# Kernel tuning notes

Hardware: AMD Instinct MI355X
Metric: run time of the kernel (lower is better)

Reference implementation:

```python
import jax, jax.numpy as jnp
import numpy as np

N = 50000      # nodes
E = 800000     # edges (before self loops)
RNA, SS, H, G = 645, 6, 128, 200
EPS = 1e-5

def setup_inputs() -> dict:
    key = jax.random.key(0)
    ks = jax.random.split(key, 16)
    def rn(k, shape, s=0.05):
        return jax.random.normal(k, shape, jnp.float32) * s
    return {
        "rna_embeddings": jax.random.normal(ks[0], (N, RNA), jnp.float32),
        "ss_emb": jax.random.normal(ks[1], (N, SS), jnp.float32),
        "edge_index": jax.random.randint(ks[2], (2, E), 0, N),
        "batch": jnp.sort(jax.random.randint(ks[3], (N,), 0, G)),
        "W_fuse": rn(ks[4], (RNA + SS, H)), "b_fuse": jnp.zeros((H,), jnp.float32),
        "ln1_g": jnp.ones((H,), jnp.float32), "ln1_b": jnp.zeros((H,), jnp.float32),
        "W_gat": rn(ks[5], (H, H)), "att_src": rn(ks[6], (H,)), "att_dst": rn(ks[7], (H,)),
        "b_gat": jnp.zeros((H,), jnp.float32),
        "gn_w": jnp.ones((H,), jnp.float32), "gn_b": jnp.zeros((H,), jnp.float32), "gn_ms": jnp.ones((H,), jnp.float32),
        "W_gate": rn(ks[8], (2 * H, H)), "b_gate": jnp.zeros((H,), jnp.float32),
        "W_head": rn(ks[9], (H, H)), "b_head": jnp.zeros((H,), jnp.float32),
        "ln2_g": jnp.ones((H,), jnp.float32), "ln2_b": jnp.zeros((H,), jnp.float32),
        "W_fc1": rn(ks[10], (H, H // 2)), "b_fc1": jnp.zeros((H // 2,), jnp.float32),
        "ln3_g": jnp.ones((H // 2,), jnp.float32), "ln3_b": jnp.zeros((H // 2,), jnp.float32),
        "W_fc2": rn(ks[11], (H // 2, 1)), "b_fc2": jnp.zeros((1,), jnp.float32),
    }

def _ln(x, g, b):
    m = jnp.mean(x, -1, keepdims=True)
    v = jnp.mean(jnp.square(x - m), -1, keepdims=True)
    return (x - m) * jax.lax.rsqrt(v + EPS) * g + b

def _graphnorm(x, batch, w, b, ms):
    cnt = jax.ops.segment_sum(jnp.ones((x.shape[0], 1), x.dtype), batch, num_segments=G)
    mean = jax.ops.segment_sum(x, batch, num_segments=G) / jnp.maximum(cnt, 1.0)
    out = x - ms * mean[batch]
    var = jax.ops.segment_sum(jnp.square(out), batch, num_segments=G) / jnp.maximum(cnt, 1.0)
    std = jnp.sqrt(var + EPS)
    return w * out / std[batch] + b

def _gat(x, src, dst, W, a_src, a_dst, bias):
    xw = x @ W                                     # [N,H]
    e = (xw @ a_src)[src] + (xw @ a_dst)[dst]      # per-edge score
    e = jax.nn.leaky_relu(e, 0.2)
    m = jax.ops.segment_max(e, dst, num_segments=N)  # every dst has a self loop
    e = jnp.exp(e - m[dst])
    s = jax.ops.segment_sum(e, dst, num_segments=N)
    alpha = e / (s[dst] + 1e-16)
    return jax.ops.segment_sum(alpha[:, None] * xw[src], dst, num_segments=N) + bias

def reference(rna_embeddings, ss_emb, edge_index, batch,
              W_fuse, b_fuse, ln1_g, ln1_b,
              W_gat, att_src, att_dst, b_gat,
              gn_w, gn_b, gn_ms,
              W_gate, b_gate, W_head, b_head, ln2_g, ln2_b,
              W_fc1, b_fc1, ln3_g, ln3_b, W_fc2, b_fc2):
    loop = jnp.arange(N)
    src = jnp.concatenate([edge_index[0], loop])   # PyG GATConv add_self_loops=True
    dst = jnp.concatenate([edge_index[1], loop])
    h = jax.nn.relu(_ln(jnp.concatenate([rna_embeddings, ss_emb], -1) @ W_fuse + b_fuse, ln1_g, ln1_b))
    h_res = h
    h = jax.nn.relu(_graphnorm(_gat(h, src, dst, W_gat, att_src, att_dst, b_gat), batch, gn_w, gn_b, gn_ms))
    h1 = h
    h = jax.nn.relu(_graphnorm(_gat(h1, src, dst, W_gat, att_src, att_dst, b_gat), batch, gn_w, gn_b, gn_ms))
    h2 = h + h_res
    gate = jax.nn.sigmoid(jnp.concatenate([h1, h2], -1) @ W_gate + b_gate)
    h = gate * h1 + (1.0 - gate) * h2
    h = jax.nn.relu(_ln(h @ W_head + b_head, ln2_g, ln2_b))
    h = jax.nn.relu(_ln(h @ W_fc1 + b_fc1, ln3_g, ln3_b))
    return (h @ W_fc2 + b_fc2)[:, 0]
```

## Files before the change

kernel.cpp:

```cpp
#include <hip/hip_runtime.h>
#include <hip/hip_bf16.h>
#include <math.h>

#define NN 50000
#define EE 800000
#define RNA_D 645
#define KFUSE 651
#define KPACK 704
#define HD 128
#define GG 200
#define SAK 72
#define HGS 136

typedef __attribute__((ext_vector_type(8))) short shortx8;
typedef __attribute__((ext_vector_type(4))) float floatx4;

__device__ __forceinline__ float lrelu(float x){ return x >= 0.f ? x : 0.2f*x; }
__device__ __forceinline__ short f2bf(float x){
  union { __hip_bfloat16 h; short s; } u; u.h = __float2bfloat16(x); return u.s;
}
__device__ __forceinline__ float bf2f(short s){
  union { float f; unsigned u; } c; c.u = ((unsigned)(unsigned short)s) << 16; return c.f;
}
__device__ __forceinline__ float2 upk(unsigned u){
  union { float f; unsigned v; } a, b;
  a.v = u << 16; b.v = u & 0xffff0000u;
  return make_float2(a.f, b.f);
}

__launch_bounds__(256)
__global__ void pack_kernel(const float* __restrict__ rna, const float* __restrict__ ss,
                            short* __restrict__ Abf){
  int row = blockIdx.x*2 + (threadIdx.x >> 7);
  int t = threadIdx.x & 127;
  if (row >= NN) return;
  const float* rrow = rna + (size_t)row*RNA_D;
  short* orow = Abf + (size_t)row*KPACK;
  #pragma unroll
  for (int j=0;j<6;++j){
    int c = t + j*128;
    if (c < KPACK){
      float v = 0.f;
      if (c < RNA_D) v = rrow[c];
      else if (c < KFUSE) v = ss[row*6 + (c - RNA_D)];
      orow[c] = f2bf(v);
    }
  }
}

__global__ void hist_gstart_kernel(const int* __restrict__ dst, int* __restrict__ deg,
                                   const int* __restrict__ batch, int* __restrict__ gstart){
  int e = blockIdx.x*256 + threadIdx.x;
  if (e < EE) atomicAdd(&deg[dst[e]], 1);
  if (e < NN){
    int g = batch[e];
    if (e == 0){ for (int gg=0; gg<=g; ++gg) gstart[gg] = 0; }
    else { int gp = batch[e-1]; for (int gg=gp+1; gg<=g; ++gg) gstart[gg] = e; }
    if (e == NN-1){ for (int gg=g+1; gg<=GG; ++gg) gstart[gg] = NN; }
  }
}
__global__ void scan1_kernel(const int* __restrict__ deg, int* __restrict__ row_start,
                             int* __restrict__ blocksum){
  __shared__ int s[256];
  int i = blockIdx.x*256 + threadIdx.x;
  int v = (i < NN) ? deg[i] : 0;
  s[threadIdx.x] = v;
  __syncthreads();
  for (int off=1; off<256; off<<=1){
    int t = (threadIdx.x >= off) ? s[threadIdx.x-off] : 0;
    __syncthreads();
    s[threadIdx.x] += t;
    __syncthreads();
  }
  if (i < NN) row_start[i] = s[threadIdx.x] - v;
  if (threadIdx.x == 255) blocksum[blockIdx.x] = s[255];
}
__global__ void scan2_kernel(int* __restrict__ blocksum, int nb){
  __shared__ int s[256];
  int v = (threadIdx.x < nb) ? blocksum[threadIdx.x] : 0;
  s[threadIdx.x] = v;
  __syncthreads();
  for (int off=1; off<256; off<<=1){
    int t = (threadIdx.x >= off) ? s[threadIdx.x-off] : 0;
    __syncthreads();
    s[threadIdx.x] += t;
    __syncthreads();
  }
  blocksum[threadIdx.x] = s[threadIdx.x] - v;
}
__global__ void scan3_kernel(int* __restrict__ row_start, const int* __restrict__ blocksum,
                             int* __restrict__ cursor){
  int i = blockIdx.x*256 + threadIdx.x;
  if (i < NN){
    int v = row_start[i] + blocksum[blockIdx.x];
    row_start[i] = v;
    cursor[i] = v;
  }
  if (i == 0) row_start[NN] = EE;
}
__global__ void scatter_kernel(const int* __restrict__ srcl, const int* __restrict__ dstl,
                               int* __restrict__ cursor, int* __restrict__ csr_src){
  int e = blockIdx.x*256 + threadIdx.x;
  if (e >= EE) return;
  int d = dstl[e];
  int slot = atomicAdd(&cursor[d], 1);
  csr_src[slot] = srcl[e];
}

__global__ void wprep_all_kernel(const float* __restrict__ Wf, const float* __restrict__ Wg,
                                 const float* __restrict__ Wgt, const float* __restrict__ Wh,
                                 const float* __restrict__ W1,
                                 short* __restrict__ Tf, short* __restrict__ Tg,
                                 short* __restrict__ Tgt, short* __restrict__ Th,
                                 short* __restrict__ T1){
  int idx = blockIdx.x*256 + threadIdx.x;
  const int S0=128*KPACK, S1=128*128, S2=128*256, S3=128*128, S4=64*128;
  if (idx < S0){ int n=idx/KPACK, k=idx-n*KPACK; Tf[idx]=f2bf(k<KFUSE ? Wf[k*128+n] : 0.f); return; }
  idx -= S0;
  if (idx < S1){ int n=idx>>7, k=idx&127; Tg[idx]=f2bf(Wg[k*128+n]); return; }
  idx -= S1;
  if (idx < S2){ int n=idx>>8, k=idx&255; Tgt[idx]=f2bf(Wgt[k*128+n]); return; }
  idx -= S2;
  if (idx < S3){ int n=idx>>7, k=idx&127; Th[idx]=f2bf(Wh[k*128+n]); return; }
  idx -= S3;
  if (idx < S4){ int n=idx>>7, k=idx&127; T1[idx]=f2bf(W1[k*64+n]); return; }
}

template<int MODE, int NT, bool GNA>
__launch_bounds__(256)
__global__ void mfma_gemm(const float* __restrict__ A0,
                          const short* __restrict__ Apk,
                          const short* __restrict__ Wt, const float* __restrict__ bias,
                          const float* __restrict__ gw, const float* __restrict__ gb,
                          const float* __restrict__ as_, const float* __restrict__ ad_,
                          const int* __restrict__ batch, const float* __restrict__ gnsh,
                          const float* __restrict__ gnsc, float* __restrict__ side,
                          float* __restrict__ out, short* __restrict__ outb,
                          float* __restrict__ es, float* __restrict__ ed,
                          int K, int Kp){
  __shared__ short sA[128*SAK];
  __shared__ short sB[NT*16*SAK];
  const int tid  = threadIdx.x;
  const int wave = tid >> 6, lane = tid & 63;
  const int quad = lane >> 4, l16 = lane & 15;
  const int rowBase = blockIdx.x * 128;
  const int NCOL = NT*16;

  floatx4 acc[2][NT];
  #pragma unroll
  for (int t=0;t<2;++t)
    #pragma unroll
    for (int ct=0;ct<NT;++ct)
      #pragma unroll
      for (int j=0;j<4;++j) acc[t][ct][j] = 0.f;

  const int srow = tid >> 1, shalf = tid & 1;
  const int sgr = rowBase + srow;

  for (int k0 = 0; k0 < K; k0 += 64){
    if (MODE == 0){
      #pragma unroll
      for (int j=0;j<4;++j){
        int flat = tid + j*256;
        int r = flat >> 3, c8 = flat & 7;
        int gr = rowBase + r;
        shortx8 v = {0,0,0,0,0,0,0,0};
        if (gr < NN) v = *(const shortx8*)&Apk[(size_t)gr*KPACK + k0 + c8*8];
        *(shortx8*)&sA[r*SAK + c8*8] = v;
      }
    } else {
      int kb = k0 + shalf*32;
      short tmp[32];
      if (GNA){
        int g = (sgr < NN) ? batch[sgr] : 0;
        const float* py  = A0 + (size_t)sgr*HD + kb;
        const float* psh = gnsh + g*HD + kb;
        const float* psc = gnsc + g*HD + kb;
        const float* pbb = gb + kb;
        #pragma unroll
        for (int q4=0;q4<8;++q4){
          float4 yv = (sgr < NN) ? *(const float4*)(py + q4*4) : make_float4(0.f,0.f,0.f,0.f);
          float4 sh = *(const float4*)(psh + q4*4);
          float4 sc = *(const float4*)(psc + q4*4);
          float4 bb = *(const float4*)(pbb + q4*4);
          float4 v;
          v.x = fmaxf((yv.x - sh.x)*sc.x + bb.x, 0.f);
          v.y = fmaxf((yv.y - sh.y)*sc.y + bb.y, 0.f);
          v.z = fmaxf((yv.z - sh.z)*sc.z + bb.z, 0.f);
          v.w = fmaxf((yv.w - sh.w)*sc.w + bb.w, 0.f);
          if (sgr < NN) *(float4*)&side[(size_t)sgr*HD + kb + q4*4] = v;
          tmp[q4*4+0]=f2bf(v.x); tmp[q4*4+1]=f2bf(v.y);
          tmp[q4*4+2]=f2bf(v.z); tmp[q4*4+3]=f2bf(v.w);
        }
      } else {
        const float* p = A0 + (size_t)sgr*HD + kb;
        #pragma unroll
        for (int q4=0;q4<8;++q4){
          float4 f = (sgr < NN) ? *(const float4*)(p + q4*4) : make_float4(0.f,0.f,0.f,0.f);
          tmp[q4*4+0]=f2bf(f.x); tmp[q4*4+1]=f2bf(f.y);
          tmp[q4*4+2]=f2bf(f.z); tmp[q4*4+3]=f2bf(f.w);
        }
      }
      #pragma unroll
      for (int q8=0;q8<4;++q8)
        *(shortx8*)&sA[srow*SAK + shalf*32 + q8*8] = *(shortx8*)&tmp[q8*8];
    }
    {
      int col = tid >> 1, kb = k0 + (tid&1)*32;
      #pragma unroll
      for (int q8=0;q8<4;++q8)
        *(shortx8*)&sB[col*SAK + (tid&1)*32 + q8*8] = *(const shortx8*)&Wt[(size_t)col*Kp + kb + q8*8];
    }
    __syncthreads();
    #pragma unroll
    for (int ks=0; ks<2; ++ks){
      int kb = ks*32 + quad*8;
      shortx8 af0 = *(const shortx8*)&sA[(wave*32 +      l16)*SAK + kb];
      shortx8 af1 = *(const shortx8*)&sA[(wave*32 + 16 + l16)*SAK + kb];
      #pragma unroll
      for (int ct=0; ct<NT; ++ct){
        shortx8 bf = *(const shortx8*)&sB[(ct*16 + l16)*SAK + kb];
        acc[0][ct] = __builtin_amdgcn_mfma_f32_16x16x32_bf16(af0, bf, acc[0][ct], 0,0,0);
        acc[1][ct] = __builtin_amdgcn_mfma_f32_16x16x32_bf16(af1, bf, acc[1][ct], 0,0,0);
      }
    }
    __syncthreads();
  }

  if (MODE == 1){
    float asv[NT], adv[NT];
    #pragma unroll
    for (int ct=0;ct<NT;++ct){ asv[ct] = as_[ct*16+l16]; adv[ct] = ad_[ct*16+l16]; }
    #pragma unroll
    for (int t=0;t<2;++t)
      #pragma unroll
      for (int i=0;i<4;++i){
        int gr = rowBase + wave*32 + t*16 + quad*4 + i;
        float s=0.f, d=0.f;
        #pragma unroll
        for (int ct=0;ct<NT;++ct){
          float v = acc[t][ct][i];
          s = fmaf(v, asv[ct], s); d = fmaf(v, adv[ct], d);
          if (gr < NN) outb[(size_t)gr*HD + ct*16 + l16] = f2bf(v);
        }
        #pragma unroll
        for (int off=1; off<16; off<<=1){ s += __shfl_xor(s,off); d += __shfl_xor(d,off); }
        if (l16 == 0 && gr < NN){ es[gr] = s; ed[gr] = d; }
      }
  } else {
    float biasv[NT], gv[NT], bv[NT];
    #pragma unroll
    for (int ct=0;ct<NT;++ct){
      biasv[ct] = bias[ct*16+l16]; gv[ct] = gw[ct*16+l16]; bv[ct] = gb[ct*16+l16];
    }
    #pragma unroll
    for (int t=0;t<2;++t)
      #pragma unroll
      for (int i=0;i<4;++i){
        int gr = rowBase + wave*32 + t*16 + quad*4 + i;
        float v[NT]; float s=0.f, q=0.f;
        #pragma unroll
        for (int ct=0;ct<NT;++ct){
          v[ct] = acc[t][ct][i] + biasv[ct];
          s += v[ct]; q = fmaf(v[ct], v[ct], q);
        }
        #pragma unroll
        for (int off=1; off<16; off<<=1){ s += __shfl_xor(s,off); q += __shfl_xor(q,off); }
        float mean = s * (1.f/NCOL);
        float inv  = rsqrtf(q*(1.f/NCOL) - mean*mean + 1e-5f);
        if (gr < NN){
          #pragma unroll
          for (int ct=0;ct<NT;++ct)
            out[(size_t)gr*NCOL + ct*16 + l16] = fmaxf((v[ct]-mean)*inv*gv[ct] + bv[ct], 0.f);
        }
      }
  }
}

__launch_bounds__(256)
__global__ void gat_aggregate_kernel(const short* __restrict__ xwb, const float* __restrict__ es,
                                     const float* __restrict__ ed, const int* __restrict__ row_start,
                                     const int* __restrict__ csr_src, const float* __restrict__ bgat,
                                     float* __restrict__ out){
  int gid = blockIdx.x*256 + threadIdx.x;
  int n = gid >> 6, lane = gid & 63;
  if (n >= NN) return;
  int beg = row_start[n], end = row_start[n+1];
  float edn = ed[n];
  float sc_self = lrelu(es[n] + edn);

  int i0 = beg + lane;
  bool v0 = i0 < end;
  int sA = v0 ? csr_src[i0] : 0;
  float eA = v0 ? lrelu(es[sA] + edn) : -3.0e38f;
  float m = fmaxf(sc_self, eA);
  for (int i = beg + 64 + lane; i < end; i += 64)
    m = fmaxf(m, lrelu(es[csr_src[i]] + edn));
  #pragma unroll
  for (int off=1; off<64; off<<=1) m = fmaxf(m, __shfl_xor(m, off));

  float wA = v0 ? __expf(eA - m) : 0.f;
  float wsum_l = wA;
  float wself = __expf(sc_self - m);
  float2 self2 = upk(*(const unsigned*)&xwb[(size_t)n*HD + 2*lane]);
  float a0 = wself*self2.x, a1 = wself*self2.y;

  int deg0 = min(end - beg, 64);
  int j = 0;
  for (; j + 8 <= deg0; j += 8){
    int ss[8]; float ww[8]; unsigned xv[8];
    #pragma unroll
    for (int u=0;u<8;++u){ ss[u]=__shfl(sA,j+u); ww[u]=__shfl(wA,j+u); }
    #pragma unroll
    for (int u=0;u<8;++u) xv[u] = *(const unsigned*)&xwb[(size_t)ss[u]*HD + 2*lane];
    #pragma unroll
    for (int u=0;u<8;++u){ float2 f=upk(xv[u]); a0=fmaf(ww[u],f.x,a0); a1=fmaf(ww[u],f.y,a1); }
  }
  for (; j < deg0; ++j){
    int s=__shfl(sA,j); float w=__shfl(wA,j);
    float2 f = upk(*(const unsigned*)&xwb[(size_t)s*HD + 2*lane]);
    a0=fmaf(w,f.x,a0); a1=fmaf(w,f.y,a1);
  }
  for (int c = beg + 64; c < end; c += 64){
    int i = c + lane;
    bool vb = i < end;
    int sB = vb ? csr_src[i] : 0;
    float wB = vb ? __expf(lrelu(es[sB] + edn) - m) : 0.f;
    wsum_l += wB;
    int degc = min(end - c, 64);
    for (int jj=0; jj<degc; ++jj){
      int s=__shfl(sB,jj); float w=__shfl(wB,jj);
      float2 f = upk(*(const unsigned*)&xwb[(size_t)s*HD + 2*lane]);
      a0=fmaf(w,f.x,a0); a1=fmaf(w,f.y,a1);
    }
  }
  #pragma unroll
  for (int off=1; off<64; off<<=1) wsum_l += __shfl_xor(wsum_l, off);
  float dinv = 1.f/(wsum_l + wself + 1e-16f);
  float2 b2 = *(const float2*)&bgat[2*lane];
  float2 o; o.x = a0*dinv + b2.x; o.y = a1*dinv + b2.y;
  *(float2*)&out[(size_t)n*HD + 2*lane] = o;
}

__launch_bounds__(256)
__global__ void gn_group_kernel(const float* __restrict__ x, const int* __restrict__ gstart,
                                const float* __restrict__ gnw, const float* __restrict__ gnms,
                                float* __restrict__ shiftv, float* __restrict__ scalev){
  int g = blockIdx.x;
  int n0 = gstart[g], n1 = gstart[g+1];
  int f = threadIdx.x & 127, half = threadIdx.x >> 7;
  float s = 0.f, q = 0.f;
  for (int n = n0 + half; n < n1; n += 2){
    float v = x[(size_t)n*HD + f];
    s += v; q = fmaf(v, v, q);
  }
  __shared__ float rs[256], rq[256];
  rs[threadIdx.x] = s; rq[threadIdx.x] = q;
  __syncthreads();
  if (threadIdx.x < 128){
    s = rs[threadIdx.x] + rs[threadIdx.x+128];
    q = rq[threadIdx.x] + rq[threadIdx.x+128];
    float c = fmaxf((float)(n1 - n0), 1.f);
    float mean = s / c;
    float ms = gnms[f];
    float var = q/c - mean*mean*ms*(2.f - ms);
    shiftv[g*HD+f] = ms*mean;
    scalev[g*HD+f] = gnw[f] / sqrtf(var + 1e-5f);
  }
}

__launch_bounds__(256)
__global__ void tail_kernel(const float* __restrict__ h1, const float* __restrict__ y2,
                            const float* __restrict__ hres, const int* __restrict__ batch,
                            const float* __restrict__ gnsh, const float* __restrict__ gnsc,
                            const float* __restrict__ gnb,
                            const short* __restrict__ Wt_gate, const float* __restrict__ b_gate,
                            const short* __restrict__ Wt_head, const float* __restrict__ b_head,
                            const float* __restrict__ ln2g, const float* __restrict__ ln2b,
                            const short* __restrict__ Wt_fc1, const float* __restrict__ b_fc1,
                            const float* __restrict__ ln3g, const float* __restrict__ ln3b,
                            const float* __restrict__ W_fc2, const float* __restrict__ b_fc2,
                            float* __restrict__ outp){
  __shared__ short hgL[128*HGS];
  __shared__ short sA[128*SAK];
  __shared__ short sB[128*SAK];
  const int tid = threadIdx.x, wave = tid>>6, lane = tid&63;
  const int quad = lane>>4, l16 = lane&15;
  const int rowBase = blockIdx.x*128;
  const int srow = tid>>1, shalf = tid&1;
  const int sgr = rowBase + srow;

  floatx4 acc[2][8];
  #pragma unroll
  for (int t=0;t<2;++t)
    #pragma unroll
    for (int ct=0;ct<8;++ct)
      #pragma unroll
      for (int j=0;j<4;++j) acc[t][ct][j]=0.f;

  for (int c2=0; c2<4; ++c2){
    int kb = c2*64 + shalf*32;
    short tmp[32];
    if (kb < 128){
      const float* p = h1 + (size_t)sgr*HD + kb;
      #pragma unroll
      for (int q4=0;q4<8;++q4){
        float4 f = (sgr < NN) ? *(const float4*)(p + q4*4) : make_float4(0.f,0.f,0.f,0.f);
        tmp[q4*4+0]=f2bf(f.x); tmp[q4*4+1]=f2bf(f.y);
        tmp[q4*4+2]=f2bf(f.z); tmp[q4*4+3]=f2bf(f.w);
      }
    } else {
      int cb = kb - 128;
      int g = (sgr < NN) ? batch[sgr] : 0;
      const float* py  = y2   + (size_t)sgr*HD + cb;
      const float* ph  = hres + (size_t)sgr*HD + cb;
      const float* psh = gnsh + g*HD + cb;
      const float* psc = gnsc + g*HD + cb;
      const float* pbb = gnb + cb;
      #pragma unroll
      for (int q4=0;q4<8;++q4){
        float4 yv = (sgr < NN) ? *(const float4*)(py + q4*4) : make_float4(0.f,0.f,0.f,0.f);
        float4 hv = (sgr < NN) ? *(const float4*)(ph + q4*4) : make_float4(0.f,0.f,0.f,0.f);
        float4 sh = *(const float4*)(psh + q4*4);
        float4 sc = *(const float4*)(psc + q4*4);
        float4 bb = *(const float4*)(pbb + q4*4);
        float4 v;
        v.x = fmaxf((yv.x - sh.x)*sc.x + bb.x, 0.f) + hv.x;
        v.y = fmaxf((yv.y - sh.y)*sc.y + bb.y, 0.f) + hv.y;
        v.z = fmaxf((yv.z - sh.z)*sc.z + bb.z, 0.f) + hv.z;
        v.w = fmaxf((yv.w - sh.w)*sc.w + bb.w, 0.f) + hv.w;
        tmp[q4*4+0]=f2bf(v.x); tmp[q4*4+1]=f2bf(v.y);
        tmp[q4*4+2]=f2bf(v.z); tmp[q4*4+3]=f2bf(v.w);
      }
      #pragma unroll
      for (int q8=0;q8<4;++q8)
        *(shortx8*)&hgL[srow*HGS + cb + q8*8] = *(shortx8*)&tmp[q8*8];
    }
    #pragma unroll
    for (int q8=0;q8<4;++q8)
      *(shortx8*)&sA[srow*SAK + shalf*32 + q8*8] = *(shortx8*)&tmp[q8*8];
    {
      int col = tid >> 1, kb2 = c2*64 + (tid&1)*32;
      #pragma unroll
      for (int q8=0;q8<4;++q8)
        *(shortx8*)&sB[col*SAK + (tid&1)*32 + q8*8] = *(const shortx8*)&Wt_gate[(size_t)col*256 + kb2 + q8*8];
    }
    __syncthreads();
    #pragma unroll
    for (int ks=0; ks<2; ++ks){
      int kk = ks*32 + quad*8;
      shortx8 af0 = *(const shortx8*)&sA[(wave*32 +      l16)*SAK + kk];
      shortx8 af1 = *(const shortx8*)&sA[(wave*32 + 16 + l16)*SAK + kk];
      #pragma unroll
      for (int ct=0; ct<8; ++ct){
        shortx8 bf = *(const shortx8*)&sB[(ct*16 + l16)*SAK + kk];
        acc[0][ct] = __builtin_amdgcn_mfma_f32_16x16x32_bf16(af0, bf, acc[0][ct], 0,0,0);
        acc[1][ct] = __builtin_amdgcn_mfma_f32_16x16x32_bf16(af1, bf, acc[1][ct], 0,0,0);
      }
    }
    __syncthreads();
  }
  {
    float biasv[8];
    #pragma unroll
    for (int ct=0;ct<8;++ct) biasv[ct] = b_gate[ct*16+l16];
    #pragma unroll
    for (int t=0;t<2;++t)
      #pragma unroll
      for (int i=0;i<4;++i){
        int row = wave*32 + t*16 + quad*4 + i;
        int gr = rowBase + row;
        #pragma unroll
        for (int ct=0;ct<8;++ct){
          int c = ct*16 + l16;
          float g = 1.f/(1.f + __expf(-(acc[t][ct][i] + biasv[ct])));
          float x1 = (gr < NN) ? h1[(size_t)gr*HD + c] : 0.f;
          float x2 = bf2f(hgL[row*HGS + c]);
          hgL[row*HGS + c] = f2bf(g*x1 + (1.f-g)*x2);
        }
      }
  }
  __syncthreads();

  floatx4 acc2[2][8];
  #pragma unroll
  for (int t=0;t<2;++t)
    #pragma unroll
    for (int ct=0;ct<8;++ct)
      #pragma unroll
      for (int j=0;j<4;++j) acc2[t][ct][j]=0.f;
  for (int c2=0;c2<2;++c2){
    {
      int col = tid >> 1, kb2 = c2*64 + (tid&1)*32;
      #pragma unroll
      for (int q8=0;q8<4;++q8)
        *(shortx8*)&sB[col*SAK + (tid&1)*32 + q8*8] = *(const shortx8*)&Wt_head[(size_t)col*128 + kb2 + q8*8];
    }
    __syncthreads();
    #pragma unroll
    for (int ks=0; ks<2; ++ks){
      int kg = c2*64 + ks*32 + quad*8;
      int kk = ks*32 + quad*8;
      shortx8 af0 = *(const shortx8*)&hgL[(wave*32 +      l16)*HGS + kg];
      shortx8 af1 = *(const shortx8*)&hgL[(wave*32 + 16 + l16)*HGS + kg];
      #pragma unroll
      for (int ct=0; ct<8; ++ct){
        shortx8 bf = *(const shortx8*)&sB[(ct*16 + l16)*SAK + kk];
        acc2[0][ct] = __builtin_amdgcn_mfma_f32_16x16x32_bf16(af0, bf, acc2[0][ct], 0,0,0);
        acc2[1][ct] = __builtin_amdgcn_mfma_f32_16x16x32_bf16(af1, bf, acc2[1][ct], 0,0,0);
      }
    }
    __syncthreads();
  }
  {
    float biasv[8], gv[8], bv[8];
    #pragma unroll
    for (int ct=0;ct<8;++ct){
      biasv[ct] = b_head[ct*16+l16]; gv[ct] = ln2g[ct*16+l16]; bv[ct] = ln2b[ct*16+l16];
    }
    #pragma unroll
    for (int t=0;t<2;++t)
      #pragma unroll
      for (int i=0;i<4;++i){
        int row = wave*32 + t*16 + quad*4 + i;
        float v[8]; float s=0.f, q=0.f;
        #pragma unroll
        for (int ct=0;ct<8;++ct){
          v[ct] = acc2[t][ct][i] + biasv[ct];
          s += v[ct]; q = fmaf(v[ct], v[ct], q);
        }
        #pragma unroll
        for (int off=1; off<16; off<<=1){ s += __shfl_xor(s,off); q += __shfl_xor(q,off); }
        float mean = s * (1.f/128.f);
        float inv  = rsqrtf(q*(1.f/128.f) - mean*mean + 1e-5f);
        #pragma unroll
        for (int ct=0;ct<8;++ct)
          hgL[row*HGS + ct*16 + l16] = f2bf(fmaxf((v[ct]-mean)*inv*gv[ct] + bv[ct], 0.f));
      }
  }
  __syncthreads();

  floatx4 acc3[2][4];
  #pragma unroll
  for (int t=0;t<2;++t)
    #pragma unroll
    for (int ct=0;ct<4;++ct)
      #pragma unroll
      for (int j=0;j<4;++j) acc3[t][ct][j]=0.f;
  for (int c2=0;c2<2;++c2){
    if (tid < 128){
      int col = tid >> 1, kb2 = c2*64 + (tid&1)*32;
      #pragma unroll
      for (int q8=0;q8<4;++q8)
        *(shortx8*)&sB[col*SAK + (tid&1)*32 + q8*8] = *(const shortx8*)&Wt_fc1[(size_t)col*128 + kb2 + q8*8];
    }
    __syncthreads();
    #pragma unroll
    for (int ks=0; ks<2; ++ks){
      int kg = c2*64 + ks*32 + quad*8;
      int kk = ks*32 + quad*8;
      shortx8 af0 = *(const shortx8*)&hgL[(wave*32 +      l16)*HGS + kg];
      shortx8 af1 = *(const shortx8*)&hgL[(wave*32 + 16 + l16)*HGS + kg];
      #pragma unroll
      for (int ct=0; ct<4; ++ct){
        shortx8 bf = *(const shortx8*)&sB[(ct*16 + l16)*SAK + kk];
        acc3[0][ct] = __builtin_amdgcn_mfma_f32_16x16x32_bf16(af0, bf, acc3[0][ct], 0,0,0);
        acc3[1][ct] = __builtin_amdgcn_mfma_f32_16x16x32_bf16(af1, bf, acc3[1][ct], 0,0,0);
      }
    }
    __syncthreads();
  }
  {
    float biasv[4], gv[4], bv[4], w2v[4];
    #pragma unroll
    for (int ct=0;ct<4;++ct){
      biasv[ct] = b_fc1[ct*16+l16]; gv[ct] = ln3g[ct*16+l16]; bv[ct] = ln3b[ct*16+l16];
      w2v[ct] = W_fc2[ct*16+l16];
    }
    float b2 = b_fc2[0];
    #pragma unroll
    for (int t=0;t<2;++t)
      #pragma unroll
      for (int i=0;i<4;++i){
        int gr = rowBase + wave*32 + t*16 + quad*4 + i;
        float v[4]; float s=0.f, q=0.f;
        #pragma unroll
        for (int ct=0;ct<4;++ct){
          v[ct] = acc3[t][ct][i] + biasv[ct];
          s += v[ct]; q = fmaf(v[ct], v[ct], q);
        }
        #pragma unroll
        for (int off=1; off<16; off<<=1){ s += __shfl_xor(s,off); q += __shfl_xor(q,off); }
        float mean = s * (1.f/64.f);
        float inv  = rsqrtf(q*(1.f/64.f) - mean*mean + 1e-5f);
        float p = 0.f;
        #pragma unroll
        for (int ct=0;ct<4;++ct){
          float o = fmaxf((v[ct]-mean)*inv*gv[ct] + bv[ct], 0.f);
          p = fmaf(o, w2v[ct], p);
        }
        #pragma unroll
        for (int off=1; off<16; off<<=1) p += __shfl_xor(p, off);
        if (l16 == 0 && gr < NN) outp[gr] = p + b2;
      }
  }
}

extern "C" void kernel_launch(void* const* d_in, const int* in_sizes, int n_in,
                              void* d_out, int out_size, void* d_ws, size_t ws_size,
                              hipStream_t stream){
  const float* rna    = (const float*)d_in[0];
  const float* ss     = (const float*)d_in[1];
  const int*   eidx   = (const int*)d_in[2];
  const int*   batch  = (const int*)d_in[3];
  const float* W_fuse = (const float*)d_in[4];
  const float* b_fuse = (const float*)d_in[5];
  const float* ln1_g  = (const float*)d_in[6];
  const float* ln1_b  = (const float*)d_in[7];
  const float* W_gat  = (const float*)d_in[8];
  const float* att_src= (const float*)d_in[9];
  const float* att_dst= (const float*)d_in[10];
  const float* b_gat  = (const float*)d_in[11];
  const float* gn_w   = (const float*)d_in[12];
  const float* gn_b   = (const float*)d_in[13];
  const float* gn_ms  = (const float*)d_in[14];
  const float* W_gate = (const float*)d_in[15];
  const float* b_gate = (const float*)d_in[16];
  const float* W_head = (const float*)d_in[17];
  const float* b_head = (const float*)d_in[18];
  const float* ln2_g  = (const float*)d_in[19];
  const float* ln2_b  = (const float*)d_in[20];
  const float* W_fc1  = (const float*)d_in[21];
  const float* b_fc1  = (const float*)d_in[22];
  const float* ln3_g  = (const float*)d_in[23];
  const float* ln3_b  = (const float*)d_in[24];
  const float* W_fc2  = (const float*)d_in[25];
  const float* b_fc2  = (const float*)d_in[26];
  float* outp = (float*)d_out;

  const int* srcl = eidx;
  const int* dstl = eidx + EE;

  char* base = (char*)d_ws;
  size_t off = 0;
  auto alloc = [&](size_t bytes)->void*{
    void* p = base + off; off = (off + bytes + 255) & ~(size_t)255; return p;
  };
  float* h    = (float*)alloc((size_t)NN*HD*4);
  float* h1   = (float*)alloc((size_t)NN*HD*4);
  float* y    = (float*)alloc((size_t)NN*HD*4);
  short* xwb  = (short*)alloc((size_t)NN*HD*2);
  float* es   = (float*)alloc((size_t)NN*4);
  float* ed   = (float*)alloc((size_t)NN*4);
  float* shiftv = (float*)alloc(GG*HD*4);
  float* scalev = (float*)alloc(GG*HD*4);
  int* deg       = (int*)alloc((size_t)NN*4);
  int* row_start = (int*)alloc((size_t)(NN+1)*4);
  int* cursor    = (int*)alloc((size_t)NN*4);
  int* csr_src   = (int*)alloc((size_t)EE*4);
  int* blocksum  = (int*)alloc(256*4);
  int* gstart    = (int*)alloc((GG+1)*4);
  short* Abf     = (short*)alloc((size_t)NN*KPACK*2);
  short* Wt_fuse = (short*)alloc((size_t)128*KPACK*2);
  short* Wt_gat  = (short*)alloc((size_t)128*128*2);
  short* Wt_gate = (short*)alloc((size_t)128*256*2);
  short* Wt_head = (short*)alloc((size_t)128*128*2);
  short* Wt_fc1  = (short*)alloc((size_t)64*128*2);

  const int NB  = (NN + 255)/256;
  const int GB  = (NN + 127)/128;
  const int EB  = (EE + 255)/256;
  const int WVB = (NN*64 + 255)/256;
  const int WPREP_TOT = 128*KPACK + 128*128 + 128*256 + 128*128 + 64*128;

  pack_kernel<<<(NN+1)/2, 256, 0, stream>>>(rna, ss, Abf);
  wprep_all_kernel<<<(WPREP_TOT+255)/256, 256, 0, stream>>>(
      W_fuse, W_gat, W_gate, W_head, W_fc1,
      Wt_fuse, Wt_gat, Wt_gate, Wt_head, Wt_fc1);

  hipMemsetAsync(deg, 0, (size_t)NN*4, stream);
  hist_gstart_kernel<<<EB, 256, 0, stream>>>(dstl, deg, batch, gstart);
  scan1_kernel<<<NB, 256, 0, stream>>>(deg, row_start, blocksum);
  scan2_kernel<<<1, 256, 0, stream>>>(blocksum, NB);
  scan3_kernel<<<NB, 256, 0, stream>>>(row_start, blocksum, cursor);
  scatter_kernel<<<EB, 256, 0, stream>>>(srcl, dstl, cursor, csr_src);

  mfma_gemm<0,8,false><<<GB, 256, 0, stream>>>(nullptr, Abf, Wt_fuse, b_fuse, ln1_g, ln1_b,
      nullptr, nullptr, nullptr, nullptr, nullptr, nullptr, h, nullptr, nullptr, nullptr, KPACK, KPACK);

  mfma_gemm<1,8,false><<<GB, 256, 0, stream>>>(h, nullptr, Wt_gat, nullptr, nullptr, nullptr,
      att_src, att_dst, nullptr, nullptr, nullptr, nullptr, nullptr, xwb, es, ed, HD, HD);
  gat_aggregate_kernel<<<WVB, 256, 0, stream>>>(xwb, es, ed, row_start, csr_src, b_gat, y);
  gn_group_kernel<<<GG, 256, 0, stream>>>(y, gstart, gn_w, gn_ms, shiftv, scalev);

  mfma_gemm<1,8,true><<<GB, 256, 0, stream>>>(y, nullptr, Wt_gat, nullptr, nullptr, gn_b,
      att_src, att_dst, batch, shiftv, scalev, h1, nullptr, xwb, es, ed, HD, HD);
  gat_aggregate_kernel<<<WVB, 256, 0, stream>>>(xwb, es, ed, row_start, csr_src, b_gat, y);
  gn_group_kernel<<<GG, 256, 0, stream>>>(y, gstart, gn_w, gn_ms, shiftv, scalev);

  tail_kernel<<<GB, 256, 0, stream>>>(h1, y, h, batch, shiftv, scalev, gn_b,
      Wt_gate, b_gate, Wt_head, b_head, ln2_g, ln2_b,
      Wt_fc1, b_fc1, ln3_g, ln3_b, W_fc2, b_fc2, outp);
}
```

Measured before the change: 623.9 us.

## Fuse input packing into fuse GEMM, store hidden states in bf16, merge scans

Drops the separate pack kernel. The fuse GEMM now reads the fp32 rna/ss inputs directly and converts them to bf16 while staging into shared memory. This removes a full write and re-read of a large packed bf16 matrix. The hidden states h and h1 are stored as bf16 instead of fp32 and consumed in bf16 by the xW GEMM and the tail kernel, which halves their traffic at some cost in precision for the residual path. The three-kernel degree scan becomes a single 1024-thread block, and the GAT aggregation tail loops are processed in padded groups of 8 gathers instead of one at a time.

```diff
diff --git a/kernel.cpp b/kernel.cpp
--- a/kernel.cpp
+++ b/kernel.cpp
@@ -28,26 +28,6 @@
   return make_float2(a.f, b.f);
 }
 
-__launch_bounds__(256)
-__global__ void pack_kernel(const float* __restrict__ rna, const float* __restrict__ ss,
-                            short* __restrict__ Abf){
-  int row = blockIdx.x*2 + (threadIdx.x >> 7);
-  int t = threadIdx.x & 127;
-  if (row >= NN) return;
-  const float* rrow = rna + (size_t)row*RNA_D;
-  short* orow = Abf + (size_t)row*KPACK;
-  #pragma unroll
-  for (int j=0;j<6;++j){
-    int c = t + j*128;
-    if (c < KPACK){
-      float v = 0.f;
-      if (c < RNA_D) v = rrow[c];
-      else if (c < KFUSE) v = ss[row*6 + (c - RNA_D)];
-      orow[c] = f2bf(v);
-    }
-  }
-}
-
 __global__ void hist_gstart_kernel(const int* __restrict__ dst, int* __restrict__ deg,
                                    const int* __restrict__ batch, int* __restrict__ gstart){
   int e = blockIdx.x*256 + threadIdx.x;
@@ -59,44 +39,25 @@
     if (e == NN-1){ for (int gg=g+1; gg<=GG; ++gg) gstart[gg] = NN; }
   }
 }
-__global__ void scan1_kernel(const int* __restrict__ deg, int* __restrict__ row_start,
-                             int* __restrict__ blocksum){
-  __shared__ int s[256];
-  int i = blockIdx.x*256 + threadIdx.x;
-  int v = (i < NN) ? deg[i] : 0;
-  s[threadIdx.x] = v;
+__launch_bounds__(1024)
+__global__ void scan_all_kernel(const int* __restrict__ deg, int* __restrict__ row_start,
+                                int* __restrict__ cursor){
+  __shared__ int s[1024];
+  int t = threadIdx.x;
+  int b0 = t*49, b1 = min(b0+49, NN);
+  int sum = 0;
+  for (int i=b0;i<b1;++i) sum += deg[i];
+  s[t] = sum;
   __syncthreads();
-  for (int off=1; off<256; off<<=1){
-    int t = (threadIdx.x >= off) ? s[threadIdx.x-off] : 0;
-    __syncthreads();
-    s[threadIdx.x] += t;
-    __syncthreads();
-  }
-  if (i < NN) row_start[i] = s[threadIdx.x] - v;
-  if (threadIdx.x == 255) blocksum[blockIdx.x] = s[255];
-}
-__global__ void scan2_kernel(int* __restrict__ blocksum, int nb){
-  __shared__ int s[256];
-  int v = (threadIdx.x < nb) ? blocksum[threadIdx.x] : 0;
-  s[threadIdx.x] = v;
-  __syncthreads();
-  for (int off=1; off<256; off<<=1){
-    int t = (threadIdx.x >= off) ? s[threadIdx.x-off] : 0;
-    __syncthreads();
-    s[threadIdx.x] += t;
-    __syncthreads();
-  }
-  blocksum[threadIdx.x] = s[threadIdx.x] - v;
-}
-__global__ void scan3_kernel(int* __restrict__ row_start, const int* __restrict__ blocksum,
-                             int* __restrict__ cursor){
-  int i = blockIdx.x*256 + threadIdx.x;
-  if (i < NN){
-    int v = row_start[i] + blocksum[blockIdx.x];
-    row_start[i] = v;
-    cursor[i] = v;
-  }
-  if (i == 0) row_start[NN] = EE;
+  for (int off=1; off<1024; off<<=1){
+    int v = (t>=off) ? s[t-off] : 0;
+    __syncthreads();
+    s[t] += v;
+    __syncthreads();
+  }
+  int pre = (t==0) ? 0 : s[t-1];
+  for (int i=b0;i<b1;++i){ int d=deg[i]; row_start[i]=pre; cursor[i]=pre; pre+=d; }
+  if (t==0) row_start[NN] = EE;
 }
 __global__ void scatter_kernel(const int* __restrict__ srcl, const int* __restrict__ dstl,
                                int* __restrict__ cursor, int* __restrict__ csr_src){
@@ -126,90 +87,45 @@
   if (idx < S4){ int n=idx>>7, k=idx&127; T1[idx]=f2bf(W1[k*64+n]); return; }
 }
 
-template<int MODE, int NT, bool GNA>
 __launch_bounds__(256)
-__global__ void mfma_gemm(const float* __restrict__ A0,
-                          const short* __restrict__ Apk,
-                          const short* __restrict__ Wt, const float* __restrict__ bias,
-                          const float* __restrict__ gw, const float* __restrict__ gb,
-                          const float* __restrict__ as_, const float* __restrict__ ad_,
-                          const int* __restrict__ batch, const float* __restrict__ gnsh,
-                          const float* __restrict__ gnsc, float* __restrict__ side,
-                          float* __restrict__ out, short* __restrict__ outb,
-                          float* __restrict__ es, float* __restrict__ ed,
-                          int K, int Kp){
+__global__ void fuse_gemm_kernel(const float* __restrict__ rna, const float* __restrict__ ss,
+                                 const short* __restrict__ Wt, const float* __restrict__ bias,
+                                 const float* __restrict__ gw, const float* __restrict__ gb,
+                                 short* __restrict__ hb){
   __shared__ short sA[128*SAK];
-  __shared__ short sB[NT*16*SAK];
+  __shared__ short sB[128*SAK];
   const int tid  = threadIdx.x;
   const int wave = tid >> 6, lane = tid & 63;
   const int quad = lane >> 4, l16 = lane & 15;
   const int rowBase = blockIdx.x * 128;
-  const int NCOL = NT*16;
-
-  floatx4 acc[2][NT];
+
+  floatx4 acc[2][8];
   #pragma unroll
   for (int t=0;t<2;++t)
     #pragma unroll
-    for (int ct=0;ct<NT;++ct)
+    for (int ct=0;ct<8;++ct)
       #pragma unroll
       for (int j=0;j<4;++j) acc[t][ct][j] = 0.f;
 
-  const int srow = tid >> 1, shalf = tid & 1;
-  const int sgr = rowBase + srow;
-
-  for (int k0 = 0; k0 < K; k0 += 64){
-    if (MODE == 0){
-      #pragma unroll
-      for (int j=0;j<4;++j){
-        int flat = tid + j*256;
-        int r = flat >> 3, c8 = flat & 7;
-        int gr = rowBase + r;
-        shortx8 v = {0,0,0,0,0,0,0,0};
-        if (gr < NN) v = *(const shortx8*)&Apk[(size_t)gr*KPACK + k0 + c8*8];
-        *(shortx8*)&sA[r*SAK + c8*8] = v;
-      }
-    } else {
-      int kb = k0 + shalf*32;
-      short tmp[32];
-      if (GNA){
-        int g = (sgr < NN) ? batch[sgr] : 0;
-        const float* py  = A0 + (size_t)sgr*HD + kb;
-        const float* psh = gnsh + g*HD + kb;
-        const float* psc = gnsc + g*HD + kb;
-        const float* pbb = gb + kb;
-        #pragma unroll
-        for (int q4=0;q4<8;++q4){
-          float4 yv = (sgr < NN) ? *(const float4*)(py + q4*4) : make_float4(0.f,0.f,0.f,0.f);
-          float4 sh = *(const float4*)(psh + q4*4);
-          float4 sc = *(const float4*)(psc + q4*4);
-          float4 bb = *(const float4*)(pbb + q4*4);
-          float4 v;
-          v.x = fmaxf((yv.x - sh.x)*sc.x + bb.x, 0.f);
-          v.y = fmaxf((yv.y - sh.y)*sc.y + bb.y, 0.f);
-          v.z = fmaxf((yv.z - sh.z)*sc.z + bb.z, 0.f);
-          v.w = fmaxf((yv.w - sh.w)*sc.w + bb.w, 0.f);
-          if (sgr < NN) *(float4*)&side[(size_t)sgr*HD + kb + q4*4] = v;
-          tmp[q4*4+0]=f2bf(v.x); tmp[q4*4+1]=f2bf(v.y);
-          tmp[q4*4+2]=f2bf(v.z); tmp[q4*4+3]=f2bf(v.w);
-        }
-      } else {
-        const float* p = A0 + (size_t)sgr*HD + kb;
-        #pragma unroll
-        for (int q4=0;q4<8;++q4){
-          float4 f = (sgr < NN) ? *(const float4*)(p + q4*4) : make_float4(0.f,0.f,0.f,0.f);
-          tmp[q4*4+0]=f2bf(f.x); tmp[q4*4+1]=f2bf(f.y);
-          tmp[q4*4+2]=f2bf(f.z); tmp[q4*4+3]=f2bf(f.w);
-        }
-      }
+  const int rsub = tid >> 6;
+  const int col  = tid & 63;
+
+  for (int k0 = 0; k0 < KPACK; k0 += 64){
+    #pragma unroll
+    for (int i=0;i<32;++i){
+      int row = i*4 + rsub;
+      int gr = rowBase + row;
+      int gk = k0 + col;
+      float v = 0.f;
+      if (gr < NN && gk < KFUSE)
+        v = (gk < RNA_D) ? rna[(size_t)gr*RNA_D + gk] : ss[gr*6 + (gk - RNA_D)];
+      sA[row*SAK + col] = f2bf(v);
+    }
+    {
+      int bcol = tid >> 1, kb = k0 + (tid&1)*32;
       #pragma unroll
       for (int q8=0;q8<4;++q8)
-        *(shortx8*)&sA[srow*SAK + shalf*32 + q8*8] = *(shortx8*)&tmp[q8*8];
-    }
-    {
-      int col = tid >> 1, kb = k0 + (tid&1)*32;
-      #pragma unroll
-      for (int q8=0;q8<4;++q8)
-        *(shortx8*)&sB[col*SAK + (tid&1)*32 + q8*8] = *(const shortx8*)&Wt[(size_t)col*Kp + kb + q8*8];
+        *(shortx8*)&sB[bcol*SAK + (tid&1)*32 + q8*8] = *(const shortx8*)&Wt[(size_t)bcol*KPACK + kb + q8*8];
     }
     __syncthreads();
     #pragma unroll
@@ -218,7 +134,7 @@
       shortx8 af0 = *(const shortx8*)&sA[(wave*32 +      l16)*SAK + kb];
       shortx8 af1 = *(const shortx8*)&sA[(wave*32 + 16 + l16)*SAK + kb];
       #pragma unroll
-      for (int ct=0; ct<NT; ++ct){
+      for (int ct=0; ct<8; ++ct){
         shortx8 bf = *(const shortx8*)&sB[(ct*16 + l16)*SAK + kb];
         acc[0][ct] = __builtin_amdgcn_mfma_f32_16x16x32_bf16(af0, bf, acc[0][ct], 0,0,0);
         acc[1][ct] = __builtin_amdgcn_mfma_f32_16x16x32_bf16(af1, bf, acc[1][ct], 0,0,0);
@@ -226,55 +142,138 @@
     }
     __syncthreads();
   }
-
-  if (MODE == 1){
-    float asv[NT], adv[NT];
-    #pragma unroll
-    for (int ct=0;ct<NT;++ct){ asv[ct] = as_[ct*16+l16]; adv[ct] = ad_[ct*16+l16]; }
-    #pragma unroll
-    for (int t=0;t<2;++t)
-      #pragma unroll
-      for (int i=0;i<4;++i){
-        int gr = rowBase + wave*32 + t*16 + quad*4 + i;
-        float s=0.f, d=0.f;
-        #pragma unroll
-        for (int ct=0;ct<NT;++ct){
-          float v = acc[t][ct][i];
-          s = fmaf(v, asv[ct], s); d = fmaf(v, adv[ct], d);
-          if (gr < NN) outb[(size_t)gr*HD + ct*16 + l16] = f2bf(v);
-        }
-        #pragma unroll
-        for (int off=1; off<16; off<<=1){ s += __shfl_xor(s,off); d += __shfl_xor(d,off); }
-        if (l16 == 0 && gr < NN){ es[gr] = s; ed[gr] = d; }
-      }
-  } else {
-    float biasv[NT], gv[NT], bv[NT];
-    #pragma unroll
-    for (int ct=0;ct<NT;++ct){
-      biasv[ct] = bias[ct*16+l16]; gv[ct] = gw[ct*16+l16]; bv[ct] = gb[ct*16+l16];
-    }
-    #pragma unroll
-    for (int t=0;t<2;++t)
-      #pragma unroll
-      for (int i=0;i<4;++i){
-        int gr = rowBase + wave*32 + t*16 + quad*4 + i;
-        float v[NT]; float s=0.f, q=0.f;
-        #pragma unroll
-        for (int ct=0;ct<NT;++ct){
-          v[ct] = acc[t][ct][i] + biasv[ct];
-          s += v[ct]; q = fmaf(v[ct], v[ct], q);
-        }
-        #pragma unroll
-        for (int off=1; off<16; off<<=1){ s += __shfl_xor(s,off); q += __shfl_xor(q,off); }
-        float mean = s * (1.f/NCOL);
-        float inv  = rsqrtf(q*(1.f/NCOL) - mean*mean + 1e-5f);
-        if (gr < NN){
-          #pragma unroll
-          for (int ct=0;ct<NT;++ct)
-            out[(size_t)gr*NCOL + ct*16 + l16] = fmaxf((v[ct]-mean)*inv*gv[ct] + bv[ct], 0.f);
-        }
-      }
-  }
+  float biasv[8], gv[8], bv[8];
+  #pragma unroll
+  for (int ct=0;ct<8;++ct){
+    biasv[ct] = bias[ct*16+l16]; gv[ct] = gw[ct*16+l16]; bv[ct] = gb[ct*16+l16];
+  }
+  #pragma unroll
+  for (int t=0;t<2;++t)
+    #pragma unroll
+    for (int i=0;i<4;++i){
+      int gr = rowBase + wave*32 + t*16 + quad*4 + i;
+      float v[8]; float s=0.f, q=0.f;
+      #pragma unroll
+      for (int ct=0;ct<8;++ct){
+        v[ct] = acc[t][ct][i] + biasv[ct];
+        s += v[ct]; q = fmaf(v[ct], v[ct], q);
+      }
+      #pragma unroll
+      for (int off=1; off<16; off<<=1){ s += __shfl_xor(s,off); q += __shfl_xor(q,off); }
+      float mean = s * (1.f/128.f);
+      float inv  = rsqrtf(q*(1.f/128.f) - mean*mean + 1e-5f);
+      if (gr < NN){
+        #pragma unroll
+        for (int ct=0;ct<8;++ct)
+          hb[(size_t)gr*HD + ct*16 + l16] = f2bf(fmaxf((v[ct]-mean)*inv*gv[ct] + bv[ct], 0.f));
+      }
+    }
+}
+
+template<bool GNA>
+__launch_bounds__(256)
+__global__ void xw_gemm_kernel(const short* __restrict__ Ab, const float* __restrict__ Af,
+                               const short* __restrict__ Wt,
+                               const float* __restrict__ as_, const float* __restrict__ ad_,
+                               const int* __restrict__ batch, const float* __restrict__ gnsh,
+                               const float* __restrict__ gnsc, const float* __restrict__ gnb,
+                               short* __restrict__ sideb,
+                               short* __restrict__ xwb, float* __restrict__ es, float* __restrict__ ed){
+  __shared__ short sA[128*SAK];
+  __shared__ short sB[128*SAK];
+  const int tid  = threadIdx.x;
+  const int wave = tid >> 6, lane = tid & 63;
+  const int quad = lane >> 4, l16 = lane & 15;
+  const int rowBase = blockIdx.x * 128;
+
+  floatx4 acc[2][8];
+  #pragma unroll
+  for (int t=0;t<2;++t)
+    #pragma unroll
+    for (int ct=0;ct<8;++ct)
+      #pragma unroll
+      for (int j=0;j<4;++j) acc[t][ct][j] = 0.f;
+
+  const int srow = tid >> 1, shalf = tid & 1;
+  const int sgr = rowBase + srow;
+
+  for (int k0 = 0; k0 < HD; k0 += 64){
+    int kb = k0 + shalf*32;
+    if (GNA){
+      short tmp[32];
+      int g = (sgr < NN) ? batch[sgr] : 0;
+      const float* py  = Af + (size_t)sgr*HD + kb;
+      const float* psh = gnsh + g*HD + kb;
+      const float* psc = gnsc + g*HD + kb;
+      const float* pbb = gnb + kb;
+      #pragma unroll
+      for (int q4=0;q4<8;++q4){
+        float4 yv = (sgr < NN) ? *(const float4*)(py + q4*4) : make_float4(0.f,0.f,0.f,0.f);
+        float4 sh = *(const float4*)(psh + q4*4);
+        float4 sc = *(const float4*)(psc + q4*4);
+        float4 bb = *(const float4*)(pbb + q4*4);
+        float4 v;
+        v.x = fmaxf((yv.x - sh.x)*sc.x + bb.x, 0.f);
+        v.y = fmaxf((yv.y - sh.y)*sc.y + bb.y, 0.f);
+        v.z = fmaxf((yv.z - sh.z)*sc.z + bb.z, 0.f);
+        v.w = fmaxf((yv.w - sh.w)*sc.w + bb.w, 0.f);
+        tmp[q4*4+0]=f2bf(v.x); tmp[q4*4+1]=f2bf(v.y);
+        tmp[q4*4+2]=f2bf(v.z); tmp[q4*4+3]=f2bf(v.w);
+      }
+      #pragma unroll
+      for (int q8=0;q8<4;++q8){
+        shortx8 t8 = *(shortx8*)&tmp[q8*8];
+        *(shortx8*)&sA[srow*SAK + shalf*32 + q8*8] = t8;
+        if (sgr < NN) *(shortx8*)&sideb[(size_t)sgr*HD + kb + q8*8] = t8;
+      }
+    } else {
+      #pragma unroll
+      for (int q8=0;q8<4;++q8){
+        shortx8 v = {0,0,0,0,0,0,0,0};
+        if (sgr < NN) v = *(const shortx8*)&Ab[(size_t)sgr*HD + kb + q8*8];
+        *(shortx8*)&sA[srow*SAK + shalf*32 + q8*8] = v;
+      }
+    }
+    {
+      int col = tid >> 1, kb2 = k0 + (tid&1)*32;
+      #pragma unroll
+      for (int q8=0;q8<4;++q8)
+        *(shortx8*)&sB[col*SAK + (tid&1)*32 + q8*8] = *(const shortx8*)&Wt[(size_t)col*HD + kb2 + q8*8];
+    }
+    __syncthreads();
+    #pragma unroll
+    for (int ks=0; ks<2; ++ks){
+      int kk = ks*32 + quad*8;
+      shortx8 af0 = *(const shortx8*)&sA[(wave*32 +      l16)*SAK + kk];
+      shortx8 af1 = *(const shortx8*)&sA[(wave*32 + 16 + l16)*SAK + kk];
+      #pragma unroll
+      for (int ct=0; ct<8; ++ct){
+        shortx8 bf = *(const shortx8*)&sB[(ct*16 + l16)*SAK + kk];
+        acc[0][ct] = __builtin_amdgcn_mfma_f32_16x16x32_bf16(af0, bf, acc[0][ct], 0,0,0);
+        acc[1][ct] = __builtin_amdgcn_mfma_f32_16x16x32_bf16(af1, bf, acc[1][ct], 0,0,0);
+      }
+    }
+    __syncthreads();
+  }
+  float asv[8], adv[8];
+  #pragma unroll
+  for (int ct=0;ct<8;++ct){ asv[ct] = as_[ct*16+l16]; adv[ct] = ad_[ct*16+l16]; }
+  #pragma unroll
+  for (int t=0;t<2;++t)
+    #pragma unroll
+    for (int i=0;i<4;++i){
+      int gr = rowBase + wave*32 + t*16 + quad*4 + i;
+      float s=0.f, d=0.f;
+      #pragma unroll
+      for (int ct=0;ct<8;++ct){
+        float v = acc[t][ct][i];
+        s = fmaf(v, asv[ct], s); d = fmaf(v, adv[ct], d);
+        if (gr < NN) xwb[(size_t)gr*HD + ct*16 + l16] = f2bf(v);
+      }
+      #pragma unroll
+      for (int off=1; off<16; off<<=1){ s += __shfl_xor(s,off); d += __shfl_xor(d,off); }
+      if (l16 == 0 && gr < NN){ es[gr] = s; ed[gr] = d; }
+    }
 }
 
 __launch_bounds__(256)
@@ -306,8 +305,7 @@
   float a0 = wself*self2.x, a1 = wself*self2.y;
 
   int deg0 = min(end - beg, 64);
-  int j = 0;
-  for (; j + 8 <= deg0; j += 8){
+  for (int j = 0; j < deg0; j += 8){
     int ss[8]; float ww[8]; unsigned xv[8];
     #pragma unroll
     for (int u=0;u<8;++u){ ss[u]=__shfl(sA,j+u); ww[u]=__shfl(wA,j+u); }
@@ -315,11 +313,6 @@
     for (int u=0;u<8;++u) xv[u] = *(const unsigned*)&xwb[(size_t)ss[u]*HD + 2*lane];
     #pragma unroll
     for (int u=0;u<8;++u){ float2 f=upk(xv[u]); a0=fmaf(ww[u],f.x,a0); a1=fmaf(ww[u],f.y,a1); }
-  }
-  for (; j < deg0; ++j){
-    int s=__shfl(sA,j); float w=__shfl(wA,j);
-    float2 f = upk(*(const unsigned*)&xwb[(size_t)s*HD + 2*lane]);
-    a0=fmaf(w,f.x,a0); a1=fmaf(w,f.y,a1);
   }
   for (int c = beg + 64; c < end; c += 64){
     int i = c + lane;
@@ -328,10 +321,14 @@
     float wB = vb ? __expf(lrelu(es[sB] + edn) - m) : 0.f;
     wsum_l += wB;
     int degc = min(end - c, 64);
-    for (int jj=0; jj<degc; ++jj){
-      int s=__shfl(sB,jj); float w=__shfl(wB,jj);
-      float2 f = upk(*(const unsigned*)&xwb[(size_t)s*HD + 2*lane]);
-      a0=fmaf(w,f.x,a0); a1=fmaf(w,f.y,a1);
+    for (int jj=0; jj<degc; jj+=8){
+      int ss[8]; float ww[8]; unsigned xv[8];
+      #pragma unroll
+      for (int u=0;u<8;++u){ ss[u]=__shfl(sB,jj+u); ww[u]=__shfl(wB,jj+u); }
+      #pragma unroll
+      for (int u=0;u<8;++u) xv[u] = *(const unsigned*)&xwb[(size_t)ss[u]*HD + 2*lane];
+      #pragma unroll
+      for (int u=0;u<8;++u){ float2 f=upk(xv[u]); a0=fmaf(ww[u],f.x,a0); a1=fmaf(ww[u],f.y,a1); }
     }
   }
   #pragma unroll
@@ -370,8 +367,8 @@
 }
 
 __launch_bounds__(256)
-__global__ void tail_kernel(const float* __restrict__ h1, const float* __restrict__ y2,
-                            const float* __restrict__ hres, const int* __restrict__ batch,
+__global__ void tail_kernel(const short* __restrict__ h1b, const float* __restrict__ y2,
+                            const short* __restrict__ hb, const int* __restrict__ batch,
                             const float* __restrict__ gnsh, const float* __restrict__ gnsc,
                             const float* __restrict__ gnb,
                             const short* __restrict__ Wt_gate, const float* __restrict__ b_gate,
@@ -400,45 +397,47 @@
 
   for (int c2=0; c2<4; ++c2){
     int kb = c2*64 + shalf*32;
-    short tmp[32];
     if (kb < 128){
-      const float* p = h1 + (size_t)sgr*HD + kb;
-      #pragma unroll
-      for (int q4=0;q4<8;++q4){
-        float4 f = (sgr < NN) ? *(const float4*)(p + q4*4) : make_float4(0.f,0.f,0.f,0.f);
-        tmp[q4*4+0]=f2bf(f.x); tmp[q4*4+1]=f2bf(f.y);
-        tmp[q4*4+2]=f2bf(f.z); tmp[q4*4+3]=f2bf(f.w);
+      #pragma unroll
+      for (int q8=0;q8<4;++q8){
+        shortx8 v = {0,0,0,0,0,0,0,0};
+        if (sgr < NN) v = *(const shortx8*)&h1b[(size_t)sgr*HD + kb + q8*8];
+        *(shortx8*)&sA[srow*SAK + shalf*32 + q8*8] = v;
       }
     } else {
       int cb = kb - 128;
+      short tmp[32];
       int g = (sgr < NN) ? batch[sgr] : 0;
-      const float* py  = y2   + (size_t)sgr*HD + cb;
-      const float* ph  = hres + (size_t)sgr*HD + cb;
+      const float* py  = y2 + (size_t)sgr*HD + cb;
+      const short* ph  = hb + (size_t)sgr*HD + cb;
       const float* psh = gnsh + g*HD + cb;
       const float* psc = gnsc + g*HD + cb;
       const float* pbb = gnb + cb;
       #pragma unroll
-      for (int q4=0;q4<8;++q4){
-        float4 yv = (sgr < NN) ? *(const float4*)(py + q4*4) : make_float4(0.f,0.f,0.f,0.f);
-        float4 hv = (sgr < NN) ? *(const float4*)(ph + q4*4) : make_float4(0.f,0.f,0.f,0.f);
-        float4 sh = *(const float4*)(psh + q4*4);
-        float4 sc = *(const float4*)(psc + q4*4);
-        float4 bb = *(const float4*)(pbb + q4*4);
-        float4 v;
-        v.x = fmaxf((yv.x - sh.x)*sc.x + bb.x, 0.f) + hv.x;
-        v.y = fmaxf((yv.y - sh.y)*sc.y + bb.y, 0.f) + hv.y;
-        v.z = fmaxf((yv.z - sh.z)*sc.z + bb.z, 0.f) + hv.z;
-        v.w = fmaxf((yv.w - sh.w)*sc.w + bb.w, 0.f) + hv.w;
-        tmp[q4*4+0]=f2bf(v.x); tmp[q4*4+1]=f2bf(v.y);
-        tmp[q4*4+2]=f2bf(v.z); tmp[q4*4+3]=f2bf(v.w);
-      }
-      #pragma unroll
-      for (int q8=0;q8<4;++q8)
-        *(shortx8*)&hgL[srow*HGS + cb + q8*8] = *(shortx8*)&tmp[q8*8];
-    }
-    #pragma unroll
-    for (int q8=0;q8<4;++q8)
-      *(shortx8*)&sA[srow*SAK + shalf*32 + q8*8] = *(shortx8*)&tmp[q8*8];
+      for (int q8=0;q8<4;++q8){
+        shortx8 hv8 = {0,0,0,0,0,0,0,0};
+        if (sgr < NN) hv8 = *(const shortx8*)(ph + q8*8);
+        #pragma unroll
+        for (int q4=0;q4<2;++q4){
+          int o4 = q8*8 + q4*4;
+          float4 yv = (sgr < NN) ? *(const float4*)(py + o4) : make_float4(0.f,0.f,0.f,0.f);
+          float4 sh = *(const float4*)(psh + o4);
+          float4 sc = *(const float4*)(psc + o4);
+          float4 bb = *(const float4*)(pbb + o4);
+          tmp[o4+0] = f2bf(fmaxf((yv.x - sh.x)*sc.x + bb.x, 0.f) + bf2f(hv8[q4*4+0]));
+          tmp[o4+1] = f2bf(fmaxf((yv.y - sh.y)*sc.y + bb.y, 0.f) + bf2f(hv8[q4*4+1]));
+          tmp[o4+2] = f2bf(fmaxf((yv.z - sh.z)*sc.z + bb.z, 0.f) + bf2f(hv8[q4*4+2]));
+          tmp[o4+3] = f2bf(fmaxf((yv.w - sh.w)*sc.w + bb.w, 0.f) + bf2f(hv8[q4*4+3]));
+        }
+      }
+      #pragma unroll
+      for (int q8=0;q8<4;++q8){
+        shortx8 t8 = *(shortx8*)&tmp[q8*8];
+        hgL[srow*HGS/8*0] = hgL[0];
+        *(shortx8*)&hgL[srow*HGS + cb + q8*8] = t8;
+        *(shortx8*)&sA[srow*SAK + shalf*32 + q8*8] = t8;
+      }
+    }
     {
       int col = tid >> 1, kb2 = c2*64 + (tid&1)*32;
       #pragma unroll
@@ -474,7 +473,7 @@
         for (int ct=0;ct<8;++ct){
           int c = ct*16 + l16;
           float g = 1.f/(1.f + __expf(-(acc[t][ct][i] + biasv[ct])));
-          float x1 = (gr < NN) ? h1[(size_t)gr*HD + c] : 0.f;
+          float x1 = (gr < NN) ? bf2f(h1b[(size_t)gr*HD + c]) : 0.f;
           float x2 = bf2f(hgL[row*HGS + c]);
           hgL[row*HGS + c] = f2bf(g*x1 + (1.f-g)*x2);
         }
@@ -646,8 +645,8 @@
   auto alloc = [&](size_t bytes)->void*{
     void* p = base + off; off = (off + bytes + 255) & ~(size_t)255; return p;
   };
-  float* h    = (float*)alloc((size_t)NN*HD*4);
-  float* h1   = (float*)alloc((size_t)NN*HD*4);
+  short* hb   = (short*)alloc((size_t)NN*HD*2);
+  short* h1b  = (short*)alloc((size_t)NN*HD*2);
   float* y    = (float*)alloc((size_t)NN*HD*4);
   short* xwb  = (short*)alloc((size_t)NN*HD*2);
   float* es   = (float*)alloc((size_t)NN*4);
@@ -658,47 +657,40 @@
   int* row_start = (int*)alloc((size_t)(NN+1)*4);
   int* cursor    = (int*)alloc((size_t)NN*4);
   int* csr_src   = (int*)alloc((size_t)EE*4);
-  int* blocksum  = (int*)alloc(256*4);
   int* gstart    = (int*)alloc((GG+1)*4);
-  short* Abf     = (short*)alloc((size_t)NN*KPACK*2);
   short* Wt_fuse = (short*)alloc((size_t)128*KPACK*2);
   short* Wt_gat  = (short*)alloc((size_t)128*128*2);
   short* Wt_gate = (short*)alloc((size_t)128*256*2);
   short* Wt_head = (short*)alloc((size_t)128*128*2);
   short* Wt_fc1  = (short*)alloc((size_t)64*128*2);
 
-  const int NB  = (NN + 255)/256;
   const int GB  = (NN + 127)/128;
   const int EB  = (EE + 255)/256;
   const int WVB = (NN*64 + 255)/256;
   const int WPREP_TOT = 128*KPACK + 128*128 + 128*256 + 128*128 + 64*128;
 
-  pack_kernel<<<(NN+1)/2, 256, 0, stream>>>(rna, ss, Abf);
   wprep_all_kernel<<<(WPREP_TOT+255)/256, 256, 0, stream>>>(
       W_fuse, W_gat, W_gate, W_head, W_fc1,
       Wt_fuse, Wt_gat, Wt_gate, Wt_head, Wt_fc1);
 
   hipMemsetAsync(deg, 0, (size_t)NN*4, stream);
   hist_gstart_kernel<<<EB, 256, 0, stream>>>(dstl, deg, batch, gstart);
-  scan1_kernel<<<NB, 256, 0, stream>>>(deg, row_start, blocksum);
-  scan2_kernel<<<1, 256, 0, stream>>>(blocksum, NB);
-  scan3_kernel<<<NB, 256, 0, stream>>>(row_start, blocksum, cursor);
+  scan_all_kernel<<<1, 1024, 0, stream>>>(deg, row_start, cursor);
   scatter_kernel<<<EB, 256, 0, stream>>>(srcl, dstl, cursor, csr_src);
 
-  mfma_gemm<0,8,false><<<GB, 256, 0, stream>>>(nullptr, Abf, Wt_fuse, b_fuse, ln1_g, ln1_b,
-      nullptr, nullptr, nullptr, nullptr, nullptr, nullptr, h, nullptr, nullptr, nullptr, KPACK, KPACK);
-
-  mfma_gemm<1,8,false><<<GB, 256, 0, stream>>>(h, nullptr, Wt_gat, nullptr, nullptr, nullptr,
-      att_src, att_dst, nullptr, nullptr, nullptr, nullptr, nullptr, xwb, es, ed, HD, HD);
+  fuse_gemm_kernel<<<GB, 256, 0, stream>>>(rna, ss, Wt_fuse, b_fuse, ln1_g, ln1_b, hb);
+
+  xw_gemm_kernel<false><<<GB, 256, 0, stream>>>(hb, nullptr, Wt_gat, att_src, att_dst,
+      nullptr, nullptr, nullptr, nullptr, nullptr, xwb, es, ed);
   gat_aggregate_kernel<<<WVB, 256, 0, stream>>>(xwb, es, ed, row_start, csr_src, b_gat, y);
   gn_group_kernel<<<GG, 256, 0, stream>>>(y, gstart, gn_w, gn_ms, shiftv, scalev);
 
-  mfma_gemm<1,8,true><<<GB, 256, 0, stream>>>(y, nullptr, Wt_gat, nullptr, nullptr, gn_b,
-      att_src, att_dst, batch, shiftv, scalev, h1, nullptr, xwb, es, ed, HD, HD);
+  xw_gemm_kernel<true><<<GB, 256, 0, stream>>>(nullptr, y, Wt_gat, att_src, att_dst,
+      batch, shiftv, scalev, gn_b, h1b, xwb, es, ed);
   gat_aggregate_kernel<<<WVB, 256, 0, stream>>>(xwb, es, ed, row_start, csr_src, b_gat, y);
   gn_group_kernel<<<GG, 256, 0, stream>>>(y, gstart, gn_w, gn_ms, shiftv, scalev);
 
-  tail_kernel<<<GB, 256, 0, stream>>>(h1, y, h, batch, shiftv, scalev, gn_b,
+  tail_kernel<<<GB, 256, 0, stream>>>(h1b, y, hb, batch, shiftv, scalev, gn_b,
       Wt_gate, b_gate, Wt_head, b_head, ln2_g, ln2_b,
       Wt_fc1, b_fc1, ln3_g, ln3_b, W_fc2, b_fc2, outp);
 }
```

Result: slower. 800.3 us (+28.3%).
